# Optimization experiments

Hardware: AMD Instinct MI355X
Metric: run time of the kernel (lower is better)

Reference implementation:

```python
import jax, jax.numpy as jnp
import numpy as np

L_SEQ = 32768
H_FEAT = 512
P_STATE = 256  # state_size // 2 (conj_sym)
LOG_DT_MIN, LOG_DT_MAX = np.log(1e-3), np.log(1e-1)


def setup_inputs() -> dict:
    key = jax.random.key(0)
    ks = jax.random.split(key, 7)
    input_sequence = jax.random.normal(ks[0], (L_SEQ, H_FEAT), dtype=jnp.float32)
    # eigenvalue real parts must be negative for stability (HiPPO-LegS-like)
    lambda_real = -jax.random.uniform(ks[1], (P_STATE,), minval=0.1, maxval=1.0, dtype=jnp.float32)
    lambda_imag = jax.random.normal(ks[2], (P_STATE,), dtype=jnp.float32) * float(np.pi)
    b = jax.random.normal(ks[3], (P_STATE, H_FEAT, 2), dtype=jnp.float32) / np.sqrt(H_FEAT)
    c = jax.random.normal(ks[4], (H_FEAT, P_STATE, 2), dtype=jnp.float32) / np.sqrt(P_STATE)
    d = jax.random.normal(ks[5], (H_FEAT,), dtype=jnp.float32)
    # log-timestep init in [log(1e-3), log(1e-1)] as in init_log_steps
    delta = (LOG_DT_MIN + jax.random.uniform(ks[6], (P_STATE, 1), dtype=jnp.float32)
             * (LOG_DT_MAX - LOG_DT_MIN))
    return {"input_sequence": input_sequence, "lambda_real": lambda_real,
            "lambda_imag": lambda_imag, "b": b, "c": c, "d": d, "delta": delta}


def _binop(e_i, e_j):
    A_i, b_i = e_i
    A_j, b_j = e_j
    return A_j * A_i, A_j * b_i + b_j


def reference(input_sequence, lambda_real, lambda_imag, b, c, d, delta):
    # assemble complex parameters (stored as real [..., 2])
    Lam = lambda_real + 1j * lambda_imag            # [P]
    B = b[..., 0] + 1j * b[..., 1]                  # [P, H]
    C = c[..., 0] + 1j * c[..., 1]                  # [H, P]
    step = jnp.exp(delta[:, 0])                     # step_rescale = 1.0
    # bilinear discretization
    BL = 1.0 / (1.0 - (step / 2.0) * Lam)
    Lam_bar = BL * (1.0 + (step / 2.0) * Lam)       # [P]
    B_bar = (BL * step)[:, None] * B                # [P, H]
    # input projection: Bu[l] = B_bar @ u[l]
    Bu = jnp.einsum('lh,ph->lp', input_sequence.astype(Lam_bar.dtype), B_bar)  # [L, P]
    L = input_sequence.shape[0]
    Lam_el = jnp.broadcast_to(Lam_bar, (L, Lam_bar.shape[0]))
    _, xs = jax.lax.associative_scan(_binop, (Lam_el, Bu))  # xs: [L, P] complex states
    # output projection (conj_sym => factor 2, real part)
    ys = 2.0 * jnp.einsum('lp,hp->lh', xs, C).real  # [L, H]
    return ys + d * input_sequence
```

## Files before the change

### kernel.cpp

```cpp
#include <hip/hip_runtime.h>
#include <cstddef>

#define L_SEQ 32768
#define H_FEAT 512
#define P_STATE 256
#define N2 512
#define CS 32
#define NCH (L_SEQ / CS)

typedef __bf16 bf16x8 __attribute__((ext_vector_type(8)));
typedef float f32x4 __attribute__((ext_vector_type(4)));

#define GLDS16(g, l) __builtin_amdgcn_global_load_lds( \
    (const __attribute__((address_space(1))) void*)(g), \
    (__attribute__((address_space(3))) void*)(l), 16, 0, 0)

__device__ __forceinline__ unsigned bf_rne(float x) {
    unsigned u = __float_as_uint(x);
    return (u + 0x7fffu + ((u >> 16) & 1u)) >> 16;
}
__device__ __forceinline__ float bf_f(unsigned bits) {
    return __uint_as_float(bits << 16);
}
__device__ __forceinline__ float2 cmul(float2 a, float2 b) {
    return make_float2(fmaf(a.x, b.x, -a.y * b.y), fmaf(a.x, b.y, a.y * b.x));
}
__device__ __forceinline__ float2 cfma(float2 a, float2 b, float2 c) {
    return make_float2(fmaf(a.x, b.x, fmaf(-a.y, b.y, c.x)),
                       fmaf(a.x, b.y, fmaf(a.y, b.x, c.y)));
}

__global__ __launch_bounds__(256) void param_kernel(
    const float* __restrict__ lr, const float* __restrict__ li,
    const float* __restrict__ b,  const float* __restrict__ c,
    const float* __restrict__ delta,
    ushort* __restrict__ W_hi, ushort* __restrict__ W_lo,
    ushort* __restrict__ C2_hi, ushort* __restrict__ C2_lo,
    float2* __restrict__ Abar)
{
    int tid = blockIdx.x * blockDim.x + threadIdx.x;

    {
        int p = tid >> 9;
        int h = tid & 511;
        float step = expf(delta[p]);
        float zr = 0.5f * step * lr[p];
        float zi = 0.5f * step * li[p];
        float dr = 1.0f - zr, di = -zi;
        float den = dr * dr + di * di;
        float blr = dr / den, bli = -di / den;
        float bbr = blr * step, bbi = bli * step;
        float b0 = b[((size_t)(p * H_FEAT + h)) * 2 + 0];
        float b1 = b[((size_t)(p * H_FEAT + h)) * 2 + 1];
        float vr = bbr * b0 - bbi * b1;
        float vi = bbr * b1 + bbi * b0;
        unsigned hr = bf_rne(vr), hl = bf_rne(vr - bf_f(hr));
        unsigned ir = bf_rne(vi), il = bf_rne(vi - bf_f(ir));
        size_t o0 = (size_t)(2 * p) * H_FEAT + h;
        size_t o1 = (size_t)(2 * p + 1) * H_FEAT + h;
        W_hi[o0] = (ushort)hr; W_lo[o0] = (ushort)hl;
        W_hi[o1] = (ushort)ir; W_lo[o1] = (ushort)il;
    }

    {
        int h2 = tid >> 8;
        int p2 = tid & 255;
        float c0 =  2.0f * c[((size_t)(h2 * P_STATE + p2)) * 2 + 0];
        float c1 = -2.0f * c[((size_t)(h2 * P_STATE + p2)) * 2 + 1];
        unsigned h0 = bf_rne(c0), l0 = bf_rne(c0 - bf_f(h0));
        unsigned h1 = bf_rne(c1), l1 = bf_rne(c1 - bf_f(h1));
        size_t o0 = (size_t)h2 * N2 + 2 * p2;
        C2_hi[o0] = (ushort)h0;     C2_lo[o0] = (ushort)l0;
        C2_hi[o0 + 1] = (ushort)h1; C2_lo[o0 + 1] = (ushort)l1;
    }

    if (tid < P_STATE) {
        int p = tid;
        float step = expf(delta[p]);
        float zr = 0.5f * step * lr[p];
        float zi = 0.5f * step * li[p];
        float dr = 1.0f - zr, di = -zi;
        float den = dr * dr + di * di;
        float blr = dr / den, bli = -di / den;
        float nr = 1.0f + zr, ni = zi;
        Abar[p] = make_float2(blr * nr - bli * ni, blr * ni + bli * nr);
    }
}

__global__ __launch_bounds__(256, 2) void gemm1(
    const float* __restrict__ A,
    const ushort* __restrict__ Bhi, const ushort* __restrict__ Blo,
    float* __restrict__ C,
    const float2* __restrict__ Abar, float2* __restrict__ ends)
{
    __shared__ ushort sh[32768];
    ushort* As_hi = sh;
    ushort* As_lo = sh + 4096;
    ushort* Bs_hi = sh + 8192;
    ushort* Bs_lo = sh + 16384;
    float*  Cs    = (float*)sh;

    const int tid = threadIdx.x;
    const int ln = tid & 63, wv = tid >> 6;
    const int bm = blockIdx.y * 128, bn = blockIdx.x * 256;
    const int m = ln & 15, q = ln >> 4;
    const int wr = (wv >> 1) * 64, wc = (wv & 1) * 128;

    f32x4 acc[4][8] = {};

    for (int k0 = 0; k0 < 512; k0 += 32) {
#pragma unroll
        for (int s = 0; s < 8; s++) {
            int t = wv * 8 + s;
            int ch = t & 15;
            int row = ch * 16 + (ln >> 2);
            const ushort* src = (t < 16 ? Bhi : Blo)
                                + (size_t)(bn + row) * 512 + k0 + (ln & 3) * 8;
            ushort* dst = (t < 16 ? Bs_hi : Bs_lo) + ch * 512 + ln * 8;
            GLDS16(src, dst);
        }
#pragma unroll
        for (int r = 0; r < 4; r++) {
            int idx = tid + r * 256;
            int row = idx >> 3;
            int c4 = (idx & 7) << 2;
            const float4 v = *(const float4*)(A + (size_t)(bm + row) * 512 + k0 + c4);
            unsigned u0 = __float_as_uint(v.x), u1 = __float_as_uint(v.y);
            unsigned u2 = __float_as_uint(v.z), u3 = __float_as_uint(v.w);
            unsigned hi01 = (u0 >> 16) | (u1 & 0xffff0000u);
            unsigned hi23 = (u2 >> 16) | (u3 & 0xffff0000u);
            float d0 = v.x - __uint_as_float(u0 & 0xffff0000u);
            float d1 = v.y - __uint_as_float(u1 & 0xffff0000u);
            float d2 = v.z - __uint_as_float(u2 & 0xffff0000u);
            float d3 = v.w - __uint_as_float(u3 & 0xffff0000u);
            unsigned lo01 = (__float_as_uint(d0) >> 16) | (__float_as_uint(d1) & 0xffff0000u);
            unsigned lo23 = (__float_as_uint(d2) >> 16) | (__float_as_uint(d3) & 0xffff0000u);
            *(uint2*)(As_hi + row * 32 + c4) = make_uint2(hi01, hi23);
            *(uint2*)(As_lo + row * 32 + c4) = make_uint2(lo01, lo23);
        }
        __syncthreads();

        bf16x8 ah[4], al[4];
#pragma unroll
        for (int i = 0; i < 4; i++) {
            ah[i] = *(const bf16x8*)(As_hi + (wr + i * 16 + m) * 32 + q * 8);
            al[i] = *(const bf16x8*)(As_lo + (wr + i * 16 + m) * 32 + q * 8);
        }
#pragma unroll
        for (int j = 0; j < 8; j++) {
            bf16x8 bh = *(const bf16x8*)(Bs_hi + (wc + j * 16 + m) * 32 + q * 8);
            bf16x8 bl = *(const bf16x8*)(Bs_lo + (wc + j * 16 + m) * 32 + q * 8);
#pragma unroll
            for (int i = 0; i < 4; i++)
                acc[i][j] = __builtin_amdgcn_mfma_f32_16x16x32_bf16(ah[i], bh, acc[i][j], 0, 0, 0);
#pragma unroll
            for (int i = 0; i < 4; i++)
                acc[i][j] = __builtin_amdgcn_mfma_f32_16x16x32_bf16(al[i], bh, acc[i][j], 0, 0, 0);
#pragma unroll
            for (int i = 0; i < 4; i++)
                acc[i][j] = __builtin_amdgcn_mfma_f32_16x16x32_bf16(ah[i], bl, acc[i][j], 0, 0, 0);
        }
        __syncthreads();
    }

#pragma unroll
    for (int i = 0; i < 4; i++)
#pragma unroll
        for (int j = 0; j < 8; j++)
#pragma unroll
            for (int r = 0; r < 4; r++) {
                int row = bm + wr + i * 16 + q * 4 + r;
                int col = bn + wc + j * 16 + m;
                C[(size_t)row * 512 + col] = acc[i][j][r];
            }

    const int p_l = tid & 127;
    const int lc  = tid >> 7;
    const float2 Aop = Abar[(bn >> 1) + p_l];
#pragma unroll
    for (int h = 0; h < 2; h++) {
        if ((wv >> 1) == h) {
#pragma unroll
            for (int i = 0; i < 4; i++)
#pragma unroll
                for (int j = 0; j < 8; j++)
#pragma unroll
                    for (int r = 0; r < 4; r++)
                        Cs[(i * 16 + q * 4 + r) * 256 + wc + j * 16 + m] = acc[i][j][r];
        }
        __syncthreads();
        {
            float2 s = make_float2(0.f, 0.f);
#pragma unroll 8
            for (int i2 = 0; i2 < 32; i2++) {
                float2 u = *(const float2*)(Cs + (lc * 32 + i2) * 256 + 2 * p_l);
                s = cfma(Aop, s, u);
            }
            ends[(size_t)((bn >> 1) + p_l) * NCH + (bm >> 5) + h * 2 + lc] = s;
        }
        __syncthreads();
    }
}

__global__ __launch_bounds__(256, 2) void gemm2(
    const float* __restrict__ Bu,
    const ushort* __restrict__ Bhi, const ushort* __restrict__ Blo,
    float* __restrict__ Cout, const float* __restrict__ U,
    const float* __restrict__ dvec,
    const float2* __restrict__ Abar, const float2* __restrict__ carries)
{
    __shared__ ushort As_hi[128 * 32], As_lo[128 * 32];
    __shared__ ushort Bs_hi[256 * 32], Bs_lo[256 * 32];
    __shared__ float  Af32[128 * 32];
    const int tid = threadIdx.x;
    const int ln = tid & 63, wv = tid >> 6;
    const int bm = blockIdx.y * 128, bn = blockIdx.x * 256;
    const int m = ln & 15, q = ln >> 4;
    const int wr = (wv >> 1) * 64, wc = (wv & 1) * 128;

    const int pl = tid & 15, sg = (tid >> 4) & 3, chk = tid >> 6;

    f32x4 acc[4][8] = {};

    for (int k0 = 0; k0 < 512; k0 += 32) {
#pragma unroll
        for (int s = 0; s < 8; s++) {
            int t = wv * 8 + s;
            int ch = t & 15;
            int row = ch * 16 + (ln >> 2);
            const ushort* src = (t < 16 ? Bhi : Blo)
                                + (size_t)(bn + row) * 512 + k0 + (ln & 3) * 8;
            ushort* dst = (t < 16 ? Bs_hi : Bs_lo) + ch * 512 + ln * 8;
            GLDS16(src, dst);
        }
#pragma unroll
        for (int r = 0; r < 4; r++) {
            int idx = tid + r * 256;
            int row = idx >> 3;
            int c4 = (idx & 7) << 2;
            GLDS16(Bu + (size_t)(bm + row) * 512 + k0 + c4, Af32 + row * 32 + c4);
        }
        __syncthreads();

        {
            const int pg = (k0 >> 1) + pl;
            const float2 Aop2 = Abar[pg];
            const float2 A2 = cmul(Aop2, Aop2);
            const float2 A4 = cmul(A2, A2);
            const float2 A8 = cmul(A4, A4);
            const int rbase = chk * 32 + sg * 8;

            float2 uv[8];
            float2 s = make_float2(0.f, 0.f);
#pragma unroll
            for (int k = 0; k < 8; k++) {
                uv[k] = *(const float2*)(Af32 + (rbase + k) * 32 + 2 * pl);
                s = cfma(Aop2, s, uv[k]);
            }
            const float2 e0 = make_float2(__shfl(s.x, pl),      __shfl(s.y, pl));
            const float2 e1 = make_float2(__shfl(s.x, pl + 16), __shfl(s.y, pl + 16));
            const float2 e2 = make_float2(__shfl(s.x, pl + 32), __shfl(s.y, pl + 32));
            float2 S = carries[(size_t)pg * NCH + (bm >> 5) + chk];
            if (sg >= 1) S = cfma(A8, S, e0);
            if (sg >= 2) S = cfma(A8, S, e1);
            if (sg >= 3) S = cfma(A8, S, e2);
#pragma unroll
            for (int k = 0; k < 8; k++) {
                S = cfma(Aop2, S, uv[k]);
                unsigned hr  = bf_rne(S.x);
                unsigned lr2 = __float_as_uint(S.x - bf_f(hr)) >> 16;
                unsigned hi_ = bf_rne(S.y);
                unsigned li2 = __float_as_uint(S.y - bf_f(hi_)) >> 16;
                const int row = rbase + k;
                *(unsigned*)(As_hi + row * 32 + 2 * pl) = hr | (hi_ << 16);
                *(unsigned*)(As_lo + row * 32 + 2 * pl) = lr2 | (li2 << 16);
            }
        }
        __syncthreads();

        bf16x8 ah[4], al[4];
#pragma unroll
        for (int i = 0; i < 4; i++) {
            ah[i] = *(const bf16x8*)(As_hi + (wr + i * 16 + m) * 32 + q * 8);
            al[i] = *(const bf16x8*)(As_lo + (wr + i * 16 + m) * 32 + q * 8);
        }
#pragma unroll
        for (int j = 0; j < 8; j++) {
            bf16x8 bh = *(const bf16x8*)(Bs_hi + (wc + j * 16 + m) * 32 + q * 8);
            bf16x8 bl = *(const bf16x8*)(Bs_lo + (wc + j * 16 + m) * 32 + q * 8);
#pragma unroll
            for (int i = 0; i < 4; i++)
                acc[i][j] = __builtin_amdgcn_mfma_f32_16x16x32_bf16(ah[i], bh, acc[i][j], 0, 0, 0);
#pragma unroll
            for (int i = 0; i < 4; i++)
                acc[i][j] = __builtin_amdgcn_mfma_f32_16x16x32_bf16(al[i], bh, acc[i][j], 0, 0, 0);
#pragma unroll
            for (int i = 0; i < 4; i++)
                acc[i][j] = __builtin_amdgcn_mfma_f32_16x16x32_bf16(ah[i], bl, acc[i][j], 0, 0, 0);
        }
        __syncthreads();
    }

#pragma unroll
    for (int i = 0; i < 4; i++)
#pragma unroll
        for (int j = 0; j < 8; j++) {
            int col = bn + wc + j * 16 + m;
            float dv = dvec[col];
#pragma unroll
            for (int r = 0; r < 4; r++) {
                int row = bm + wr + i * 16 + q * 4 + r;
                Cout[(size_t)row * 512 + col] =
                    acc[i][j][r] + dv * U[(size_t)row * 512 + col];
            }
        }
}

__global__ __launch_bounds__(1024) void scan_pass2(
    const float2* __restrict__ ends, const float2* __restrict__ Abar,
    float2* __restrict__ carries)
{
    __shared__ float2 sA[NCH];
    __shared__ float2 sB[NCH];
    int p = blockIdx.x;
    int t = threadIdx.x;

    float2 a = Abar[p];
#pragma unroll
    for (int i = 0; i < 5; i++) {
        float nr = a.x * a.x - a.y * a.y;
        float ni = 2.f * a.x * a.y;
        a = make_float2(nr, ni);
    }
    float2 A = a;
    float2 bv = ends[(size_t)p * NCH + t];
    sA[t] = A; sB[t] = bv;
    __syncthreads();

    for (int off = 1; off < NCH; off <<= 1) {
        float2 pa, pb;
        bool act = (t >= off);
        if (act) { pa = sA[t - off]; pb = sB[t - off]; }
        __syncthreads();
        if (act) {
            float2 nA = make_float2(A.x * pa.x - A.y * pa.y,
                                    A.x * pa.y + A.y * pa.x);
            float2 nB = make_float2(fmaf(A.x, pb.x, fmaf(-A.y, pb.y, bv.x)),
                                    fmaf(A.x, pb.y, fmaf(A.y, pb.x, bv.y)));
            A = nA; bv = nB;
            sA[t] = A; sB[t] = bv;
        }
        __syncthreads();
    }

    float2 carry = (t == 0) ? make_float2(0.f, 0.f) : sB[t - 1];
    carries[(size_t)p * NCH + t] = carry;
}

extern "C" void kernel_launch(void* const* d_in, const int* in_sizes, int n_in,
                              void* d_out, int out_size, void* d_ws, size_t ws_size,
                              hipStream_t stream) {
    const float* u     = (const float*)d_in[0];
    const float* lr    = (const float*)d_in[1];
    const float* li    = (const float*)d_in[2];
    const float* b     = (const float*)d_in[3];
    const float* c     = (const float*)d_in[4];
    const float* dvec  = (const float*)d_in[5];
    const float* delta = (const float*)d_in[6];
    float* out = (float*)d_out;

    char* p = (char*)d_ws;
    float*  Bu      = (float*)p;   p += (size_t)L_SEQ * N2 * 4;
    float2* ends    = (float2*)p;  p += (size_t)P_STATE * NCH * 8;
    float2* carries = (float2*)p;  p += (size_t)P_STATE * NCH * 8;
    ushort* W_hi    = (ushort*)p;  p += (size_t)N2 * H_FEAT * 2;
    ushort* W_lo    = (ushort*)p;  p += (size_t)N2 * H_FEAT * 2;
    ushort* C2_hi   = (ushort*)p;  p += (size_t)H_FEAT * N2 * 2;
    ushort* C2_lo   = (ushort*)p;  p += (size_t)H_FEAT * N2 * 2;
    float2* Abar    = (float2*)p;  p += (size_t)P_STATE * 8;

    param_kernel<<<(P_STATE * H_FEAT) / 256, 256, 0, stream>>>(
        lr, li, b, c, delta, W_hi, W_lo, C2_hi, C2_lo, Abar);

    {
        dim3 grid(N2 / 256, L_SEQ / 128);
        gemm1<<<grid, 256, 0, stream>>>(u, W_hi, W_lo, Bu, Abar, ends);
    }

    scan_pass2<<<P_STATE, NCH, 0, stream>>>(ends, Abar, carries);

    {
        dim3 grid(H_FEAT / 256, L_SEQ / 128);
        gemm2<<<grid, 256, 0, stream>>>(Bu, C2_hi, C2_lo, out, u, dvec,
                                        Abar, carries);
    }
}
```

Baseline: 235.0 us.

## Overlap B-tile DMA with scan by register-staging Bu and split waitcnts

Bu and the carry and Abar values are now loaded into registers before the B-tile global_load_lds is issued, and Bu is written to LDS from registers. The first barrier waits only on those loads (vmcnt(8)), so the in-flight B-tile DMA overlaps the intra-chunk scan. The serial recurrence for the final states is also replaced with independent power-based updates (S*A^k + local prefix), shortening the dependency chain. This adds register pressure and relies on hand-placed waitcnt and sched_barrier ordering, which is fragile if the compiler reorders memory operations.

```diff
diff --git a/kernel.cpp b/kernel.cpp
--- a/kernel.cpp
+++ b/kernel.cpp
@@ -14,6 +14,8 @@
 #define GLDS16(g, l) __builtin_amdgcn_global_load_lds( \
     (const __attribute__((address_space(1))) void*)(g), \
     (__attribute__((address_space(3))) void*)(l), 16, 0, 0)
+
+#define SCHED_FENCE() __builtin_amdgcn_sched_barrier(0)
 
 __device__ __forceinline__ unsigned bf_rne(float x) {
     unsigned u = __float_as_uint(x);
@@ -223,6 +225,19 @@
     f32x4 acc[4][8] = {};
 
     for (int k0 = 0; k0 < 512; k0 += 32) {
+        const int pg = (k0 >> 1) + pl;
+        float2 S = carries[(size_t)pg * NCH + (bm >> 5) + chk];
+        float2 Aop2 = Abar[pg];
+        SCHED_FENCE();
+        float4 av[4];
+#pragma unroll
+        for (int r = 0; r < 4; r++) {
+            int idx = tid + r * 256;
+            int row = idx >> 3;
+            int c4 = (idx & 7) << 2;
+            av[r] = *(const float4*)(Bu + (size_t)(bm + row) * 512 + k0 + c4);
+        }
+        SCHED_FENCE();
 #pragma unroll
         for (int s = 0; s < 8; s++) {
             int t = wv * 8 + s;
@@ -233,50 +248,58 @@
             ushort* dst = (t < 16 ? Bs_hi : Bs_lo) + ch * 512 + ln * 8;
             GLDS16(src, dst);
         }
+        SCHED_FENCE();
 #pragma unroll
         for (int r = 0; r < 4; r++) {
             int idx = tid + r * 256;
             int row = idx >> 3;
             int c4 = (idx & 7) << 2;
-            GLDS16(Bu + (size_t)(bm + row) * 512 + k0 + c4, Af32 + row * 32 + c4);
-        }
-        __syncthreads();
+            *(float4*)(Af32 + row * 32 + c4) = av[r];
+        }
+        asm volatile("s_waitcnt vmcnt(8) lgkmcnt(0)" ::: "memory");
+        SCHED_FENCE();
+        __builtin_amdgcn_s_barrier();
+        SCHED_FENCE();
 
         {
-            const int pg = (k0 >> 1) + pl;
-            const float2 Aop2 = Abar[pg];
             const float2 A2 = cmul(Aop2, Aop2);
             const float2 A4 = cmul(A2, A2);
             const float2 A8 = cmul(A4, A4);
             const int rbase = chk * 32 + sg * 8;
 
-            float2 uv[8];
+            float2 lv[8];
             float2 s = make_float2(0.f, 0.f);
 #pragma unroll
             for (int k = 0; k < 8; k++) {
-                uv[k] = *(const float2*)(Af32 + (rbase + k) * 32 + 2 * pl);
-                s = cfma(Aop2, s, uv[k]);
+                const float2 uvv = *(const float2*)(Af32 + (rbase + k) * 32 + 2 * pl);
+                s = cfma(Aop2, s, uvv);
+                lv[k] = s;
             }
             const float2 e0 = make_float2(__shfl(s.x, pl),      __shfl(s.y, pl));
             const float2 e1 = make_float2(__shfl(s.x, pl + 16), __shfl(s.y, pl + 16));
             const float2 e2 = make_float2(__shfl(s.x, pl + 32), __shfl(s.y, pl + 32));
-            float2 S = carries[(size_t)pg * NCH + (bm >> 5) + chk];
             if (sg >= 1) S = cfma(A8, S, e0);
             if (sg >= 2) S = cfma(A8, S, e1);
             if (sg >= 3) S = cfma(A8, S, e2);
+            float2 pw = Aop2;
 #pragma unroll
             for (int k = 0; k < 8; k++) {
-                S = cfma(Aop2, S, uv[k]);
-                unsigned hr  = bf_rne(S.x);
-                unsigned lr2 = __float_as_uint(S.x - bf_f(hr)) >> 16;
-                unsigned hi_ = bf_rne(S.y);
-                unsigned li2 = __float_as_uint(S.y - bf_f(hi_)) >> 16;
+                const float sr = fmaf(pw.x, S.x, fmaf(-pw.y, S.y, lv[k].x));
+                const float si = fmaf(pw.x, S.y, fmaf(pw.y, S.x, lv[k].y));
+                unsigned hr  = bf_rne(sr);
+                unsigned lr2 = __float_as_uint(sr - bf_f(hr)) >> 16;
+                unsigned hi_ = bf_rne(si);
+                unsigned li2 = __float_as_uint(si - bf_f(hi_)) >> 16;
                 const int row = rbase + k;
                 *(unsigned*)(As_hi + row * 32 + 2 * pl) = hr | (hi_ << 16);
                 *(unsigned*)(As_lo + row * 32 + 2 * pl) = lr2 | (li2 << 16);
+                pw = cmul(pw, Aop2);
             }
         }
-        __syncthreads();
+        asm volatile("s_waitcnt vmcnt(0) lgkmcnt(0)" ::: "memory");
+        SCHED_FENCE();
+        __builtin_amdgcn_s_barrier();
+        SCHED_FENCE();
 
         bf16x8 ah[4], al[4];
 #pragma unroll
```

Result: no change. 232.3 us (median of 2 runs) (-1.1%).
